# Kernel optimization log

Hardware: AMD Instinct MI355X
Metric: run time of the kernel (lower is better)

## Reference

```python
import jax, jax.numpy as jnp
import numpy as np

B, L, H, E = 4, 2048, 8, 64
WINDOW = 8
DILATION = 1


def setup_inputs() -> dict:
    key = jax.random.key(0)
    kq, kk, kv, ka = jax.random.split(key, 4)
    queries = jax.random.normal(kq, (B, L, H, E), dtype=jnp.float32)
    keys = jax.random.normal(kk, (B, L, H, E), dtype=jnp.float32)
    values = jax.random.normal(kv, (B, L, H, E), dtype=jnp.float32)
    alpha = jax.random.uniform(ka, (1,), dtype=jnp.float32)
    return {"queries": queries, "keys": keys, "values": values, "alpha": alpha}


def _full_attention(q, k, v, scale):
    # q,k,v: [B, L, H, E]
    scores = jnp.einsum('blhe,bshe->bhls', q, k) * scale  # [B,H,L,L]
    A = jax.nn.softmax(scores, axis=-1)
    return jnp.einsum('bhls,bshd->blhd', A, v)


def _local_attention(q, k, v, scale):
    # efficient gather-based local window attention, non-causal
    Lk = k.shape[1]
    offsets = jnp.arange(-WINDOW, WINDOW + 1) * DILATION
    idx = jnp.clip(jnp.arange(Lk)[:, None] + offsets[None, :], 0, Lk - 1)
    K_win = k[:, idx]
    V_win = v[:, idx]
    scores = jnp.einsum('blhe,blwhe->blhw', q, K_win) * scale
    A = jax.nn.softmax(scores, axis=-1)
    return jnp.einsum('blhw,blwhe->blhe', A, V_win)


def reference(queries, keys, values, alpha):
    scale = 1.0 / np.sqrt(queries.shape[-1]).astype(np.float32)
    out_full = _full_attention(queries, keys, values, scale)
    out_local = _local_attention(queries, keys, values, scale)
    w = jax.nn.sigmoid(alpha[0])
    # only_target_first=True: positions 1..L-1 take out_full, position 0 is gated
    out = out_full.at[:, 0].set(w * out_full[:, 0] + (1.0 - w) * out_local[:, 0])
    return out
```

## Files before the change

kernel.cpp:

```cpp
#include <hip/hip_runtime.h>

typedef unsigned short u16;
typedef unsigned int   u32;
typedef __attribute__((ext_vector_type(8))) short short8;
typedef __attribute__((ext_vector_type(16))) float f32x16;

#define MFMA32(a, b, c) __builtin_amdgcn_mfma_f32_32x32x16_bf16(a, b, c, 0, 0, 0)

constexpr int Lv = 2048, Hv = 8, Ev = 64, HE = Hv * Ev;
constexpr float QSCALE = 0.18033688011112042f;

__device__ __forceinline__ float bf2f(u16 u) {
    u32 x = ((u32)u) << 16;
    return __builtin_bit_cast(float, x);
}
__device__ __forceinline__ u16 f2bf(float f) {
    u32 x = __builtin_bit_cast(u32, f);
    u32 r = ((x >> 16) & 1u) + 0x7fffu;
    return (u16)((x + r) >> 16);
}
__device__ __forceinline__ u32 pkbf(float a, float b) {
#if __has_builtin(__builtin_amdgcn_cvt_pk_bf16_f32)
    typedef __attribute__((ext_vector_type(2))) __bf16 bf16x2;
    bf16x2 v = __builtin_amdgcn_cvt_pk_bf16_f32(a, b);
    return __builtin_bit_cast(u32, v);
#else
    return (u32)f2bf(a) | ((u32)f2bf(b) << 16);
#endif
}
__device__ __forceinline__ float fexp2(float x) {
#if __has_builtin(__builtin_amdgcn_exp2f)
    return __builtin_amdgcn_exp2f(x);
#else
    return exp2f(x);
#endif
}

__device__ __forceinline__ int detect_isbf16(const u32* q32, int lane) {
    u32 w0 = q32[2 * lane];
    u32 w1 = q32[2 * lane + 1];
    u16 uu[4] = { (u16)(w0 & 0xffff), (u16)(w0 >> 16),
                  (u16)(w1 & 0xffff), (u16)(w1 >> 16) };
    int p = 0, z = 0;
#pragma unroll
    for (int j = 0; j < 4; ++j) {
        u16 mgn = (u16)(uu[j] & 0x7fff);
        int ex  = mgn >> 7;
        bool zero = (mgn == 0);
        bool pl   = zero || (ex >= 115 && ex <= 132);
        p += pl ? 1 : 0;
        if ((j & 1) == 0) z += zero ? 1 : 0;
    }
    int acc = p | (z << 16);
#pragma unroll
    for (int o = 1; o < 64; o <<= 1) acc += __shfl_xor(acc, o);
    int ps = acc & 0xffff, zs = acc >> 16;
    if (zs >= 100) return 0;
    return (ps >= 240) ? 1 : 0;
}

__device__ __forceinline__ short8 cvt8s(const float* p, float s) {
    float4 a = *(const float4*)p, b4 = *(const float4*)(p + 4);
    u32 r[4] = { pkbf(a.x * s, a.y * s), pkbf(a.z * s, a.w * s),
                 pkbf(b4.x * s, b4.y * s), pkbf(b4.z * s, b4.w * s) };
    return *(short8*)r;
}

__device__ __forceinline__ f32x16 zv16() {
    f32x16 z;
#pragma unroll
    for (int r = 0; r < 16; ++r) z[r] = 0.f;
    return z;
}

__device__ __forceinline__ void plswap(u32& a, u32& b) {
#if __has_builtin(__builtin_amdgcn_permlane32_swap)
    auto r = __builtin_amdgcn_permlane32_swap(a, b, false, false);
    a = r[0]; b = r[1];
#else
    int lane = (int)(threadIdx.x & 63);
    u32 ax = (u32)__shfl_xor((int)a, 32);
    u32 bx = (u32)__shfl_xor((int)b, 32);
    bool hi = lane >= 32;
    u32 na = hi ? bx : a;
    u32 nb = hi ? b  : ax;
    a = na; b = nb;
#endif
}

template <int ISBF>
__device__ __forceinline__ void attn_impl(
    const void* __restrict__ qv, const void* __restrict__ kv,
    const void* __restrict__ vv, const void* __restrict__ alphav,
    void* __restrict__ outv, u16* SMEM)
{
    const int tid  = threadIdx.x;
    const int w    = tid >> 6;
    const int lane = tid & 63;
    const int l31  = lane & 31;
    const int hi   = lane >> 5;
    const int qg   = w & 3;
    const int g    = w >> 2;

    const int fid = blockIdx.x;
    const int bh  = (fid & 7) * 4 + ((fid >> 3) & 3);
    const int rb  = fid >> 5;
    const int b   = bh >> 3, h = bh & 7;
    const int row0 = rb * 128;

    const size_t bhoff = (size_t)b * Lv * HE + h * Ev;
    const u16*   q16 = (const u16*)qv + bhoff;
    const u16*   k16 = (const u16*)kv + bhoff;
    const u16*   v16 = (const u16*)vv + bhoff;
    const float* q32 = (const float*)qv + bhoff;
    const float* k32 = (const float*)kv + bhoff;
    const float* v32 = (const float*)vv + bhoff;

    u16* Klds = SMEM;
    u16* Vt   = SMEM + 8192;

    short8 qf[4];
    {
        size_t ro = (size_t)(row0 + qg * 32 + l31) * HE + hi * 8;
        if (ISBF) {
#pragma unroll
            for (int c = 0; c < 4; ++c) {
                short8 t = *(const short8*)(q16 + ro + 16 * c);
#pragma unroll
                for (int j = 0; j < 8; ++j)
                    qf[c][j] = (short)f2bf(bf2f((u16)t[j]) * QSCALE);
            }
        } else {
#pragma unroll
            for (int c = 0; c < 4; ++c) qf[c] = cvt8s(q32 + ro + 16 * c, QSCALE);
        }
    }

    f32x16 O[2];
    O[0] = zv16(); O[1] = zv16();
    float psum = 0.f;

    const int kkey = tid >> 3, ksl = tid & 7;
    const int koff = kkey * HE + ((ksl ^ (kkey & 7)) * 8);
    const int eq = tid & 15, pp = tid >> 4;
    const int kcv = pp >> 2, pq = pp & 3;

    float4 kfaA, kfbA, vfaA, vfbA, kfaB, kfbB, vfaB, vfbB;
    uint4  kruA, kruB; uint2 vru0A, vru1A, vru0B, vru1B;

#define LOAD_TILE(S, KT)                                                       \
    do {                                                                       \
        size_t kb_ = (size_t)(KT) * 64 * HE;                                   \
        if (ISBF) {                                                            \
            kru##S  = *(const uint4*)(k16 + kb_ + koff);                       \
            const u16* vp_ = v16 + kb_ + (size_t)(2 * pp) * HE + eq * 4;       \
            vru0##S = *(const uint2*)vp_;                                      \
            vru1##S = *(const uint2*)(vp_ + HE);                               \
        } else {                                                               \
            const float* kp_ = k32 + kb_ + koff;                               \
            kfa##S = *(const float4*)kp_;                                      \
            kfb##S = *(const float4*)(kp_ + 4);                                \
            const float* vp_ = v32 + kb_ + (size_t)(2 * pp) * HE + eq * 4;     \
            vfa##S = *(const float4*)vp_;                                      \
            vfb##S = *(const float4*)(vp_ + HE);                               \
        }                                                                      \
    } while (0)

#define STORE_TILE(S, KB, VB)                                                  \
    do {                                                                       \
        if (ISBF) {                                                            \
            *(uint4*)&(KB)[tid * 8] = kru##S;                                  \
            const u16* a0_ = (const u16*)&vru0##S;                             \
            const u16* a1_ = (const u16*)&vru1##S;                             \
            _Pragma("unroll")                                                  \
            for (int j = 0; j < 4; ++j) {                                      \
                int e_  = eq * 4 + j;                                          \
                int sl_ = kcv ^ ((e_ + (e_ >> 3)) & 7);                        \
                u32 val_ = (u32)a0_[j] | ((u32)a1_[j] << 16);                  \
                *(u32*)&(VB)[e_ * 64 + sl_ * 8 + pq * 2] = val_;               \
            }                                                                  \
        } else {                                                               \
            u32 kk_[4] = { pkbf(kfa##S.x, kfa##S.y), pkbf(kfa##S.z, kfa##S.w), \
                           pkbf(kfb##S.x, kfb##S.y), pkbf(kfb##S.z, kfb##S.w) };\
            *(uint4*)&(KB)[tid * 8] = *(uint4*)kk_;                            \
            float t0_[4] = {vfa##S.x, vfa##S.y, vfa##S.z, vfa##S.w};           \
            float t1_[4] = {vfb##S.x, vfb##S.y, vfb##S.z, vfb##S.w};           \
            _Pragma("unroll")                                                  \
            for (int j = 0; j < 4; ++j) {                                      \
                int e_  = eq * 4 + j;                                          \
                int sl_ = kcv ^ ((e_ + (e_ >> 3)) & 7);                        \
                *(u32*)&(VB)[e_ * 64 + sl_ * 8 + pq * 2] = pkbf(t0_[j], t1_[j]);\
            }                                                                  \
        }                                                                      \
    } while (0)

#define BODY(KT, SL, SS)                                                       \
    do {                                                                       \
        u16* Kb = Klds + ((KT) & 1) * 4096;                                    \
        u16* Vb = Vt   + ((KT) & 1) * 4096;                                    \
        if ((KT) < 30) LOAD_TILE(SL, (KT) + 2);                                \
        f32x16 St = zv16();                                                    \
        __builtin_amdgcn_s_setprio(1);                                         \
        _Pragma("unroll")                                                      \
        for (int c = 0; c < 4; ++c) {                                          \
            int sl = (2 * c + hi) ^ (l31 & 7);                                 \
            short8 kf = *(const short8*)&Kb[(g * 32 + l31) * 64 + sl * 8];     \
            St = MFMA32(kf, qf[c], St);                                        \
        }                                                                      \
        __builtin_amdgcn_s_setprio(0);                                         \
        _Pragma("unroll")                                                      \
        for (int r = 0; r < 16; ++r) St[r] = fexp2(St[r]);       \
        _Pragma("unroll")                                                      \
        for (int r = 0; r < 16; ++r) psum += St[r];                            \
        u32 c8[8];                                                             \
        _Pragma("unroll")                                                      \
        for (int q = 0; q < 8; ++q) c8[q] = pkbf(St[2 * q], St[2 * q + 1]);    \
        _Pragma("unroll")                                                      \
        for (int t = 0; t < 2; ++t) {                                          \
            u32 a0 = c8[4 * t + 0], a1 = c8[4 * t + 1];                        \
            u32 a2 = c8[4 * t + 2], a3 = c8[4 * t + 3];                        \
            plswap(a0, a2);                                                    \
            plswap(a1, a3);                                                    \
            u32 pw_[4] = { a0, a1, a2, a3 };                                   \
            short8 pa = *(short8*)pw_;                                         \
            int ks = 2 * g + t;                                                \
            __builtin_amdgcn_s_setprio(1);                                     \
            _Pragma("unroll")                                                  \
            for (int et = 0; et < 2; ++et) {                                   \
                int e  = et * 32 + l31;                                        \
                int sl = (2 * ks + hi) ^ ((e + (e >> 3)) & 7);                 \
                short8 vf = *(const short8*)&Vb[e * 64 + sl * 8];              \
                O[et] = MFMA32(pa, vf, O[et]);                                 \
            }                                                                  \
            __builtin_amdgcn_s_setprio(0);                                     \
        }                                                                      \
        if ((KT) < 31) {                                                       \
            u16* Kn = Klds + (((KT) + 1) & 1) * 4096;                          \
            u16* Vn = Vt   + (((KT) + 1) & 1) * 4096;                          \
            STORE_TILE(SS, Kn, Vn);                                            \
            asm volatile("s_waitcnt lgkmcnt(0)" ::: "memory");                 \
            __builtin_amdgcn_s_barrier();                                      \
        }                                                                      \
    } while (0)

    LOAD_TILE(A, 0);
    LOAD_TILE(B, 1);
    STORE_TILE(A, Klds, Vt);
    asm volatile("s_waitcnt lgkmcnt(0)" ::: "memory");
    __builtin_amdgcn_s_barrier();

    for (int kt2 = 0; kt2 < 16; ++kt2) {
        const int kt = 2 * kt2;
        BODY(kt,     A, B);
        BODY(kt + 1, B, A);
    }
#undef LOAD_TILE
#undef STORE_TILE
#undef BODY

    __syncthreads();
    float pst = psum + __shfl_xor(psum, 32);
    float* cb = (float*)SMEM;
    const int cbase = qg * 2368 + lane * 36;

    if (g == 1) {
        union { f32x16 v; float4 q4[4]; } u;
        u.v = O[0];
#pragma unroll
        for (int i = 0; i < 4; ++i) *(float4*)&cb[cbase + 4 * i] = u.q4[i];
        u.v = O[1];
#pragma unroll
        for (int i = 0; i < 4; ++i) *(float4*)&cb[cbase + 16 + 4 * i] = u.q4[i];
        cb[qg * 2368 + 2304 + lane] = pst;
    }

    float locv[2] = {0.f, 0.f};
    float wgt = 0.f;
    const bool w0blk = (rb == 0) && (w == 0);
    if (w0blk) {
        const int e = lane;
        const size_t base = bhoff + e;
#define LDIN(p, i) (ISBF ? bf2f(((const u16*)(p))[i]) : ((const float*)(p))[i])
        float qe = LDIN(qv, base);
        float s[9];
#pragma unroll
        for (int j = 0; j < 9; ++j) {
            float prod = qe * LDIN(kv, base + (size_t)j * HE);
#pragma unroll
            for (int o = 1; o < 64; o <<= 1) prod += __shfl_xor(prod, o);
            s[j] = prod * 0.125f;
        }
        float mx = s[0];
#pragma unroll
        for (int j = 1; j < 9; ++j) mx = fmaxf(mx, s[j]);
        float we[9];
#pragma unroll
        for (int j = 0; j < 9; ++j) we[j] = expf(s[j] - mx);
        float denom = 9.f * we[0];
        float acc   = 9.f * we[0] * LDIN(vv, base);
#pragma unroll
        for (int j = 1; j < 9; ++j) {
            denom += we[j];
            acc   += we[j] * LDIN(vv, base + (size_t)j * HE);
        }
        float loc = acc / denom;

        float a;
        if (ISBF) {
            a = bf2f(((const u16*)alphav)[0]);
            if (!(a >= 0.0f && a <= 1.0f)) {
                float af = ((const float*)alphav)[0];
                if (af >= 0.0f && af <= 1.0f) a = af;
            }
        } else {
            a = ((const float*)alphav)[0];
            if (!(a >= 0.0f && a <= 1.0f)) {
                float ab = bf2f(((const u16*)alphav)[0]);
                if (ab >= 0.0f && ab <= 1.0f) a = ab;
            }
        }
        wgt = 1.f / (1.f + expf(-a));
#pragma unroll
        for (int et = 0; et < 2; ++et) locv[et] = __shfl(loc, et * 32 + l31);
#undef LDIN
    }

    __syncthreads();
    if (g != 0) return;

    float pstp = cb[qg * 2368 + 2304 + lane];
#pragma unroll
    for (int r = 0; r < 16; ++r) {
        O[0][r] += cb[cbase + r];
        O[1][r] += cb[cbase + 16 + r];
    }
    float invv = 1.0f / (pst + pstp);

#pragma unroll
    for (int rg = 0; rg < 4; ++rg) {
#pragma unroll
        for (int rr = 0; rr < 4; ++rr) {
            const int reg = rg * 4 + rr;
            const int rl  = rr + 8 * rg + 4 * hi;
            float inv = __shfl(invv, rl);
            int row = row0 + qg * 32 + rl;
            size_t oo = (size_t)(b * Lv + row) * HE + h * Ev + l31;
            bool blend = w0blk && (rl == 0);
#pragma unroll
            for (int et = 0; et < 2; ++et) {
                float res = O[et][reg] * inv;
                if (blend) res = wgt * res + (1.f - wgt) * locv[et];
                if (ISBF) ((u16*)outv)[oo + et * 32] = f2bf(res);
                else      ((float*)outv)[oo + et * 32] = res;
            }
        }
    }
}

__global__ __launch_bounds__(512, 4) void attn_kernel(
    const void* __restrict__ qv, const void* __restrict__ kv,
    const void* __restrict__ vv, const void* __restrict__ alphav,
    void* __restrict__ outv)
{
    __shared__ u16 SMEM[18944];

    const int isbf = detect_isbf16((const u32*)qv, threadIdx.x & 63);
    if (isbf) attn_impl<1>(qv, kv, vv, alphav, outv, SMEM);
    else      attn_impl<0>(qv, kv, vv, alphav, outv, SMEM);
}

extern "C" void kernel_launch(void* const* d_in, const int* in_sizes, int n_in,
                              void* d_out, int out_size, void* d_ws, size_t ws_size,
                              hipStream_t stream) {
    hipLaunchKernelGGL(attn_kernel, dim3(512), dim3(512), 0, stream,
                       d_in[0], d_in[1], d_in[2], d_in[3], d_out);
}
```

Before: 143.2 us.

## Software-pipeline QK of next tile with softmax/PV of previous using triple-buffered LDS

```diff
diff --git a/kernel.cpp b/kernel.cpp
--- a/kernel.cpp
+++ b/kernel.cpp
@@ -117,7 +117,7 @@
     const float* v32 = (const float*)vv + bhoff;
 
     u16* Klds = SMEM;
-    u16* Vt   = SMEM + 8192;
+    u16* Vt   = SMEM + 12288;
 
     short8 qf[4];
     {
@@ -138,6 +138,7 @@
 
     f32x16 O[2];
     O[0] = zv16(); O[1] = zv16();
+    f32x16 StA = zv16(), StB = zv16();
     float psum = 0.f;
 
     const int kkey = tid >> 3, ksl = tid & 7;
@@ -145,76 +146,81 @@
     const int eq = tid & 15, pp = tid >> 4;
     const int kcv = pp >> 2, pq = pp & 3;
 
-    float4 kfaA, kfbA, vfaA, vfbA, kfaB, kfbB, vfaB, vfbB;
-    uint4  kruA, kruB; uint2 vru0A, vru1A, vru0B, vru1B;
-
-#define LOAD_TILE(S, KT)                                                       \
+    float4 kfa, kfb, vfa, vfb;
+    uint4  kru; uint2 vru0, vru1;
+
+#define LOAD_TILE(KT)                                                          \
     do {                                                                       \
         size_t kb_ = (size_t)(KT) * 64 * HE;                                   \
         if (ISBF) {                                                            \
-            kru##S  = *(const uint4*)(k16 + kb_ + koff);                       \
+            kru  = *(const uint4*)(k16 + kb_ + koff);                          \
             const u16* vp_ = v16 + kb_ + (size_t)(2 * pp) * HE + eq * 4;       \
-            vru0##S = *(const uint2*)vp_;                                      \
-            vru1##S = *(const uint2*)(vp_ + HE);                               \
+            vru0 = *(const uint2*)vp_;                                         \
+            vru1 = *(const uint2*)(vp_ + HE);                                  \
         } else {                                                               \
             const float* kp_ = k32 + kb_ + koff;                               \
-            kfa##S = *(const float4*)kp_;                                      \
-            kfb##S = *(const float4*)(kp_ + 4);                                \
+            kfa = *(const float4*)kp_;                                         \
+            kfb = *(const float4*)(kp_ + 4);                                   \
             const float* vp_ = v32 + kb_ + (size_t)(2 * pp) * HE + eq * 4;     \
-            vfa##S = *(const float4*)vp_;                                      \
-            vfb##S = *(const float4*)(vp_ + HE);                               \
+            vfa = *(const float4*)vp_;                                         \
+            vfb = *(const float4*)(vp_ + HE);                                  \
         }                                                                      \
     } while (0)
 
-#define STORE_TILE(S, KB, VB)                                                  \
-    do {                                                                       \
+#define STORE_TILE(BS)                                                         \
+    do {                                                                       \
+        u16* KB = Klds + (BS) * 4096;                                          \
+        u16* VB = Vt   + (BS) * 4096;                                          \
         if (ISBF) {                                                            \
-            *(uint4*)&(KB)[tid * 8] = kru##S;                                  \
-            const u16* a0_ = (const u16*)&vru0##S;                             \
-            const u16* a1_ = (const u16*)&vru1##S;                             \
+            *(uint4*)&KB[tid * 8] = kru;                                       \
+            const u16* a0_ = (const u16*)&vru0;                                \
+            const u16* a1_ = (const u16*)&vru1;                                \
             _Pragma("unroll")                                                  \
             for (int j = 0; j < 4; ++j) {                                      \
                 int e_  = eq * 4 + j;                                          \
                 int sl_ = kcv ^ ((e_ + (e_ >> 3)) & 7);                        \
                 u32 val_ = (u32)a0_[j] | ((u32)a1_[j] << 16);                  \
-                *(u32*)&(VB)[e_ * 64 + sl_ * 8 + pq * 2] = val_;               \
+                *(u32*)&VB[e_ * 64 + sl_ * 8 + pq * 2] = val_;                 \
             }                                                                  \
         } else {                                                               \
-            u32 kk_[4] = { pkbf(kfa##S.x, kfa##S.y), pkbf(kfa##S.z, kfa##S.w), \
-                           pkbf(kfb##S.x, kfb##S.y), pkbf(kfb##S.z, kfb##S.w) };\
-            *(uint4*)&(KB)[tid * 8] = *(uint4*)kk_;                            \
-            float t0_[4] = {vfa##S.x, vfa##S.y, vfa##S.z, vfa##S.w};           \
-            float t1_[4] = {vfb##S.x, vfb##S.y, vfb##S.z, vfb##S.w};           \
+            u32 kk_[4] = { pkbf(kfa.x, kfa.y), pkbf(kfa.z, kfa.w),             \
+                           pkbf(kfb.x, kfb.y), pkbf(kfb.z, kfb.w) };           \
+            *(uint4*)&KB[tid * 8] = *(uint4*)kk_;                              \
+            float t0_[4] = {vfa.x, vfa.y, vfa.z, vfa.w};                       \
+            float t1_[4] = {vfb.x, vfb.y, vfb.z, vfb.w};                       \
             _Pragma("unroll")                                                  \
             for (int j = 0; j < 4; ++j) {                                      \
                 int e_  = eq * 4 + j;                                          \
                 int sl_ = kcv ^ ((e_ + (e_ >> 3)) & 7);                        \
-                *(u32*)&(VB)[e_ * 64 + sl_ * 8 + pq * 2] = pkbf(t0_[j], t1_[j]);\
+                *(u32*)&VB[e_ * 64 + sl_ * 8 + pq * 2] = pkbf(t0_[j], t1_[j]); \
             }                                                                  \
         }                                                                      \
     } while (0)
 
-#define BODY(KT, SL, SS)                                                       \
-    do {                                                                       \
-        u16* Kb = Klds + ((KT) & 1) * 4096;                                    \
-        u16* Vb = Vt   + ((KT) & 1) * 4096;                                    \
-        if ((KT) < 30) LOAD_TILE(SL, (KT) + 2);                                \
-        f32x16 St = zv16();                                                    \
+#define QK_ST(ST, BQ)                                                          \
+    do {                                                                       \
+        const u16* Kb = Klds + (BQ) * 4096;                                    \
+        (ST) = zv16();                                                         \
         __builtin_amdgcn_s_setprio(1);                                         \
         _Pragma("unroll")                                                      \
         for (int c = 0; c < 4; ++c) {                                          \
             int sl = (2 * c + hi) ^ (l31 & 7);                                 \
             short8 kf = *(const short8*)&Kb[(g * 32 + l31) * 64 + sl * 8];     \
-            St = MFMA32(kf, qf[c], St);                                        \
+            (ST) = MFMA32(kf, qf[c], (ST));                                    \
         }                                                                      \
         __builtin_amdgcn_s_setprio(0);                                         \
+    } while (0)
+
+#define FIN_ST(SP, BP)                                                         \
+    do {                                                                       \
+        const u16* Vb = Vt + (BP) * 4096;                                      \
         _Pragma("unroll")                                                      \
-        for (int r = 0; r < 16; ++r) St[r] = fexp2(St[r]);       \
+        for (int r = 0; r < 16; ++r) (SP)[r] = fexp2((SP)[r]);                 \
         _Pragma("unroll")                                                      \
-        for (int r = 0; r < 16; ++r) psum += St[r];                            \
+        for (int r = 0; r < 16; ++r) psum += (SP)[r];                          \
         u32 c8[8];                                                             \
         _Pragma("unroll")                                                      \
-        for (int q = 0; q < 8; ++q) c8[q] = pkbf(St[2 * q], St[2 * q + 1]);    \
+        for (int q = 0; q < 8; ++q) c8[q] = pkbf((SP)[2 * q], (SP)[2 * q + 1]);\
         _Pragma("unroll")                                                      \
         for (int t = 0; t < 2; ++t) {                                          \
             u32 a0 = c8[4 * t + 0], a1 = c8[4 * t + 1];                        \
@@ -234,28 +240,50 @@
             }                                                                  \
             __builtin_amdgcn_s_setprio(0);                                     \
         }                                                                      \
-        if ((KT) < 31) {                                                       \
-            u16* Kn = Klds + (((KT) + 1) & 1) * 4096;                          \
-            u16* Vn = Vt   + (((KT) + 1) & 1) * 4096;                          \
-            STORE_TILE(SS, Kn, Vn);                                            \
-            asm volatile("s_waitcnt lgkmcnt(0)" ::: "memory");                 \
-            __builtin_amdgcn_s_barrier();                                      \
-        }                                                                      \
-    } while (0)
-
-    LOAD_TILE(A, 0);
-    LOAD_TILE(B, 1);
-    STORE_TILE(A, Klds, Vt);
-    asm volatile("s_waitcnt lgkmcnt(0)" ::: "memory");
-    __builtin_amdgcn_s_barrier();
-
-    for (int kt2 = 0; kt2 < 16; ++kt2) {
-        const int kt = 2 * kt2;
-        BODY(kt,     A, B);
-        BODY(kt + 1, B, A);
-    }
+    } while (0)
+
+#define ENDBAR()                                                               \
+    do {                                                                       \
+        asm volatile("s_waitcnt lgkmcnt(0)" ::: "memory");                     \
+        __builtin_amdgcn_s_barrier();                                          \
+    } while (0)
+
+#define BODY(KT, BQ, BP, BS, SC, SP)                                           \
+    do {                                                                       \
+        LOAD_TILE((KT) + 1);                                                   \
+        QK_ST(SC, BQ);                                                         \
+        FIN_ST(SP, BP);                                                        \
+        STORE_TILE(BS);                                                        \
+        ENDBAR();                                                              \
+    } while (0)
+
+    LOAD_TILE(0);
+    STORE_TILE(0);
+    ENDBAR();
+
+    LOAD_TILE(1);
+    QK_ST(StA, 0);
+    STORE_TILE(1);
+    ENDBAR();
+
+    for (int j = 0; j < 5; ++j) {
+        const int kt = 6 * j + 1;
+        BODY(kt + 0, 1, 0, 2, StB, StA);
+        BODY(kt + 1, 2, 1, 0, StA, StB);
+        BODY(kt + 2, 0, 2, 1, StB, StA);
+        BODY(kt + 3, 1, 0, 2, StA, StB);
+        BODY(kt + 4, 2, 1, 0, StB, StA);
+        BODY(kt + 5, 0, 2, 1, StA, StB);
+    }
+
+    QK_ST(StB, 1);
+    FIN_ST(StA, 0);
+    FIN_ST(StB, 1);
 #undef LOAD_TILE
 #undef STORE_TILE
+#undef QK_ST
+#undef FIN_ST
+#undef ENDBAR
 #undef BODY
 
     __syncthreads();
@@ -362,7 +390,7 @@
     const void* __restrict__ vv, const void* __restrict__ alphav,
     void* __restrict__ outv)
 {
-    __shared__ u16 SMEM[18944];
+    __shared__ u16 SMEM[24576];
 
     const int isbf = detect_isbf16((const u32*)qv, threadIdx.x & 63);
     if (isbf) attn_impl<1>(qv, kv, vv, alphav, outv, SMEM);
```

New measurement: 152.6 us. 6.6% more time.

## Pre-convert K/V to swizzled bf16 workspace and use per-wave private LDS tiles

Applied to the files above, without the earlier changes.

```diff
diff --git a/kernel.cpp b/kernel.cpp
--- a/kernel.cpp
+++ b/kernel.cpp
@@ -9,6 +9,8 @@
 
 constexpr int Lv = 2048, Hv = 8, Ev = 64, HE = Hv * Ev;
 constexpr float QSCALE = 0.18033688011112042f;
+constexpr size_t WSV_OFF = 32u * 64u * 2048u;
+#define WS_NEED ((size_t)16777216)
 
 __device__ __forceinline__ float bf2f(u16 u) {
     u32 x = ((u32)u) << 16;
@@ -89,10 +91,56 @@
 }
 
 template <int ISBF>
+__device__ __forceinline__ void convert_impl(const void* kin, const void* vin,
+                                             u16* __restrict__ ws) {
+    const int blk = blockIdx.x;
+    const int bh  = blk >> 6, tg = blk & 63;
+    const int b   = bh >> 3,  h  = bh & 7;
+    const size_t inb = (size_t)b * Lv * HE + h * Ev;
+    u16* kimg = ws + (size_t)blk * 2048;
+    u16* vimg = ws + WSV_OFF + (size_t)blk * 2048;
+    const int t = threadIdx.x;
+#pragma unroll
+    for (int r = 0; r < 4; ++r) {
+        const int i = t + 256 * r;
+        const int a = 2 * i;
+        {
+            int key = a >> 6;
+            int slotf = (a & 63) >> 3, j0 = a & 7;
+            int e0 = ((slotf ^ (key & 7)) << 3) + j0;
+            size_t s = inb + (size_t)(tg * 32 + key) * HE + e0;
+            u32 val;
+            if (ISBF) { const u16* p = (const u16*)kin + s; val = (u32)p[0] | ((u32)p[1] << 16); }
+            else      { const float* p = (const float*)kin + s; val = pkbf(p[0], p[1]); }
+            *(u32*)&kimg[a] = val;
+        }
+        {
+            int e = a >> 5;
+            int slotf = (a & 31) >> 3, j0 = a & 7;
+            int k0 = ((slotf ^ ((e + (e >> 3)) & 3)) << 3) + j0;
+            size_t s0 = inb + (size_t)(tg * 32 + k0) * HE + e;
+            u32 val;
+            if (ISBF) { const u16* p = (const u16*)vin; val = (u32)p[s0] | ((u32)p[s0 + HE] << 16); }
+            else      { const float* p = (const float*)vin; val = pkbf(p[s0], p[s0 + HE]); }
+            *(u32*)&vimg[a] = val;
+        }
+    }
+}
+
+__global__ __launch_bounds__(256) void convert_kernel(
+    const void* __restrict__ qv, const void* __restrict__ kv,
+    const void* __restrict__ vv, u16* __restrict__ ws)
+{
+    const int isbf = detect_isbf16((const u32*)qv, threadIdx.x & 63);
+    if (isbf) convert_impl<1>(kv, vv, ws);
+    else      convert_impl<0>(kv, vv, ws);
+}
+
+template <int ISBF, int WS>
 __device__ __forceinline__ void attn_impl(
     const void* __restrict__ qv, const void* __restrict__ kv,
     const void* __restrict__ vv, const void* __restrict__ alphav,
-    void* __restrict__ outv, u16* SMEM)
+    void* __restrict__ outv, const u16* __restrict__ ws, u16* SMEM)
 {
     const int tid  = threadIdx.x;
     const int w    = tid >> 6;
@@ -116,8 +164,8 @@
     const float* k32 = (const float*)kv + bhoff;
     const float* v32 = (const float*)vv + bhoff;
 
-    u16* Klds = SMEM;
-    u16* Vt   = SMEM + 8192;
+    u16* ldsK = SMEM + w * 4096;
+    u16* ldsV = ldsK + 2048;
 
     short8 qf[4];
     {
@@ -140,123 +188,177 @@
     O[0] = zv16(); O[1] = zv16();
     float psum = 0.f;
 
-    const int kkey = tid >> 3, ksl = tid & 7;
-    const int koff = kkey * HE + ((ksl ^ (kkey & 7)) * 8);
-    const int eq = tid & 15, pp = tid >> 4;
-    const int kcv = pp >> 2, pq = pp & 3;
-
-    float4 kfaA, kfbA, vfaA, vfbA, kfaB, kfbB, vfaB, vfbB;
-    uint4  kruA, kruB; uint2 vru0A, vru1A, vru0B, vru1B;
-
-#define LOAD_TILE(S, KT)                                                       \
-    do {                                                                       \
-        size_t kb_ = (size_t)(KT) * 64 * HE;                                   \
+    const u16* kimg0 = ws + ((size_t)bh * 64 + g * 32) * 2048;
+    const u16* vimg0 = ws + WSV_OFF + ((size_t)bh * 64 + g * 32) * 2048;
+    const size_t keybase = (size_t)g * 1024;
+
+    const int k0l = lane >> 3;
+    const int kj  = lane & 7;
+    const int e0K = ((kj ^ k0l) << 3);
+    const int eoV = kj * 8;
+
+    uint4  kr0, kr1, kr2, kr3;
+    float4 fpa, fpb, fpc, fpd;
+    uint4  upa, upb;
+
+#define LK1(KT) do { const u16* ib_ = kimg0 + (size_t)(KT) * 2048 + lane * 8;  \
+        kr0 = *(const uint4*)ib_;        kr1 = *(const uint4*)(ib_ + 512);     \
+        kr2 = *(const uint4*)(ib_ + 1024); kr3 = *(const uint4*)(ib_ + 1536); } while (0)
+#define SK1() do { *(uint4*)&ldsK[lane * 8] = kr0;                             \
+        *(uint4*)&ldsK[512 + lane * 8] = kr1;                                  \
+        *(uint4*)&ldsK[1024 + lane * 8] = kr2;                                 \
+        *(uint4*)&ldsK[1536 + lane * 8] = kr3; } while (0)
+#define LV1(KT) do { const u16* ib_ = vimg0 + (size_t)(KT) * 2048 + lane * 8;  \
+        kr0 = *(const uint4*)ib_;        kr1 = *(const uint4*)(ib_ + 512);     \
+        kr2 = *(const uint4*)(ib_ + 1024); kr3 = *(const uint4*)(ib_ + 1536); } while (0)
+#define SV1() do { *(uint4*)&ldsV[lane * 8] = kr0;                             \
+        *(uint4*)&ldsV[512 + lane * 8] = kr1;                                  \
+        *(uint4*)&ldsV[1024 + lane * 8] = kr2;                                 \
+        *(uint4*)&ldsV[1536 + lane * 8] = kr3; } while (0)
+
+#define LK0(KT, CH) do {                                                       \
+        size_t tb_ = (keybase + (size_t)(KT) * 32) * HE;                       \
+        int key_ = (CH) * 16 + k0l;                                            \
         if (ISBF) {                                                            \
-            kru##S  = *(const uint4*)(k16 + kb_ + koff);                       \
-            const u16* vp_ = v16 + kb_ + (size_t)(2 * pp) * HE + eq * 4;       \
-            vru0##S = *(const uint2*)vp_;                                      \
-            vru1##S = *(const uint2*)(vp_ + HE);                               \
+            const u16* p_ = k16 + tb_ + (size_t)key_ * HE + e0K;               \
+            upa = *(const uint4*)p_;                                           \
+            upb = *(const uint4*)(p_ + 8 * HE);                                \
         } else {                                                               \
-            const float* kp_ = k32 + kb_ + koff;                               \
-            kfa##S = *(const float4*)kp_;                                      \
-            kfb##S = *(const float4*)(kp_ + 4);                                \
-            const float* vp_ = v32 + kb_ + (size_t)(2 * pp) * HE + eq * 4;     \
-            vfa##S = *(const float4*)vp_;                                      \
-            vfb##S = *(const float4*)(vp_ + HE);                               \
-        }                                                                      \
-    } while (0)
-
-#define STORE_TILE(S, KB, VB)                                                  \
-    do {                                                                       \
+            const float* p_ = k32 + tb_ + (size_t)key_ * HE + e0K;             \
+            fpa = *(const float4*)p_;            fpb = *(const float4*)(p_ + 4);\
+            fpc = *(const float4*)(p_ + 8 * HE); fpd = *(const float4*)(p_ + 8 * HE + 4);\
+        }                                                                      \
+    } while (0)
+#define SK0(CH) do {                                                           \
         if (ISBF) {                                                            \
-            *(uint4*)&(KB)[tid * 8] = kru##S;                                  \
-            const u16* a0_ = (const u16*)&vru0##S;                             \
-            const u16* a1_ = (const u16*)&vru1##S;                             \
+            *(uint4*)&ldsK[((CH)*2    ) * 512 + lane * 8] = upa;               \
+            *(uint4*)&ldsK[((CH)*2 + 1) * 512 + lane * 8] = upb;               \
+        } else {                                                               \
+            u32 t0_[4] = { pkbf(fpa.x, fpa.y), pkbf(fpa.z, fpa.w),             \
+                           pkbf(fpb.x, fpb.y), pkbf(fpb.z, fpb.w) };           \
+            u32 t1_[4] = { pkbf(fpc.x, fpc.y), pkbf(fpc.z, fpc.w),             \
+                           pkbf(fpd.x, fpd.y), pkbf(fpd.z, fpd.w) };           \
+            *(uint4*)&ldsK[((CH)*2    ) * 512 + lane * 8] = *(uint4*)t0_;      \
+            *(uint4*)&ldsK[((CH)*2 + 1) * 512 + lane * 8] = *(uint4*)t1_;      \
+        }                                                                      \
+    } while (0)
+
+#define LV0(KT, VH) do {                                                       \
+        size_t tb_ = (keybase + (size_t)(KT) * 32 + (VH) * 16 + 2 * k0l) * HE; \
+        if (ISBF) {                                                            \
+            const u16* p_ = v16 + tb_ + eoV;                                   \
+            upa = *(const uint4*)p_;                                           \
+            upb = *(const uint4*)(p_ + HE);                                    \
+        } else {                                                               \
+            const float* p_ = v32 + tb_ + eoV;                                 \
+            fpa = *(const float4*)p_;       fpb = *(const float4*)(p_ + 4);    \
+            fpc = *(const float4*)(p_ + HE); fpd = *(const float4*)(p_ + HE + 4);\
+        }                                                                      \
+    } while (0)
+#define SV0(VH) do {                                                           \
+        int s_ = (k0l >> 2) + (VH) * 2;                                        \
+        if (ISBF) {                                                            \
+            const u16* a0_ = (const u16*)&upa;                                 \
+            const u16* a1_ = (const u16*)&upb;                                 \
             _Pragma("unroll")                                                  \
-            for (int j = 0; j < 4; ++j) {                                      \
-                int e_  = eq * 4 + j;                                          \
-                int sl_ = kcv ^ ((e_ + (e_ >> 3)) & 7);                        \
-                u32 val_ = (u32)a0_[j] | ((u32)a1_[j] << 16);                  \
-                *(u32*)&(VB)[e_ * 64 + sl_ * 8 + pq * 2] = val_;               \
+            for (int j = 0; j < 8; ++j) {                                      \
+                int e_ = eoV + j;                                              \
+                int sl_ = s_ ^ ((e_ + (e_ >> 3)) & 3);                         \
+                *(u32*)&ldsV[e_ * 32 + sl_ * 8 + ((2 * k0l) & 7)] =            \
+                    (u32)a0_[j] | ((u32)a1_[j] << 16);                         \
             }                                                                  \
         } else {                                                               \
-            u32 kk_[4] = { pkbf(kfa##S.x, kfa##S.y), pkbf(kfa##S.z, kfa##S.w), \
-                           pkbf(kfb##S.x, kfb##S.y), pkbf(kfb##S.z, kfb##S.w) };\
-            *(uint4*)&(KB)[tid * 8] = *(uint4*)kk_;                            \
-            float t0_[4] = {vfa##S.x, vfa##S.y, vfa##S.z, vfa##S.w};           \
-            float t1_[4] = {vfb##S.x, vfb##S.y, vfb##S.z, vfb##S.w};           \
+            float t0_[8] = {fpa.x, fpa.y, fpa.z, fpa.w, fpb.x, fpb.y, fpb.z, fpb.w};\
+            float t1_[8] = {fpc.x, fpc.y, fpc.z, fpc.w, fpd.x, fpd.y, fpd.z, fpd.w};\
             _Pragma("unroll")                                                  \
-            for (int j = 0; j < 4; ++j) {                                      \
-                int e_  = eq * 4 + j;                                          \
-                int sl_ = kcv ^ ((e_ + (e_ >> 3)) & 7);                        \
-                *(u32*)&(VB)[e_ * 64 + sl_ * 8 + pq * 2] = pkbf(t0_[j], t1_[j]);\
+            for (int j = 0; j < 8; ++j) {                                      \
+                int e_ = eoV + j;                                              \
+                int sl_ = s_ ^ ((e_ + (e_ >> 3)) & 3);                         \
+                *(u32*)&ldsV[e_ * 32 + sl_ * 8 + ((2 * k0l) & 7)] =            \
+                    pkbf(t0_[j], t1_[j]);                                      \
             }                                                                  \
         }                                                                      \
     } while (0)
 
-#define BODY(KT, SL, SS)                                                       \
-    do {                                                                       \
-        u16* Kb = Klds + ((KT) & 1) * 4096;                                    \
-        u16* Vb = Vt   + ((KT) & 1) * 4096;                                    \
-        if ((KT) < 30) LOAD_TILE(SL, (KT) + 2);                                \
-        f32x16 St = zv16();                                                    \
+    f32x16 St;
+#define QK_() do {                                                             \
+        St = zv16();                                                           \
         __builtin_amdgcn_s_setprio(1);                                         \
         _Pragma("unroll")                                                      \
         for (int c = 0; c < 4; ++c) {                                          \
             int sl = (2 * c + hi) ^ (l31 & 7);                                 \
-            short8 kf = *(const short8*)&Kb[(g * 32 + l31) * 64 + sl * 8];     \
+            short8 kf = *(const short8*)&ldsK[l31 * 64 + sl * 8];              \
             St = MFMA32(kf, qf[c], St);                                        \
         }                                                                      \
         __builtin_amdgcn_s_setprio(0);                                         \
+    } while (0)
+
+    u32 c8[8];
+#define SM_() do {                                                             \
         _Pragma("unroll")                                                      \
-        for (int r = 0; r < 16; ++r) St[r] = fexp2(St[r]);       \
+        for (int r = 0; r < 16; ++r) St[r] = fexp2(St[r]);                     \
         _Pragma("unroll")                                                      \
         for (int r = 0; r < 16; ++r) psum += St[r];                            \
-        u32 c8[8];                                                             \
         _Pragma("unroll")                                                      \
         for (int q = 0; q < 8; ++q) c8[q] = pkbf(St[2 * q], St[2 * q + 1]);    \
+    } while (0)
+
+#define PV_(T) do {                                                            \
+        u32 a0 = c8[4 * (T) + 0], a1 = c8[4 * (T) + 1];                        \
+        u32 a2 = c8[4 * (T) + 2], a3 = c8[4 * (T) + 3];                        \
+        plswap(a0, a2);                                                        \
+        plswap(a1, a3);                                                        \
+        u32 pw_[4] = { a0, a1, a2, a3 };                                       \
+        short8 pa = *(short8*)pw_;                                             \
+        __builtin_amdgcn_s_setprio(1);                                         \
         _Pragma("unroll")                                                      \
-        for (int t = 0; t < 2; ++t) {                                          \
-            u32 a0 = c8[4 * t + 0], a1 = c8[4 * t + 1];                        \
-            u32 a2 = c8[4 * t + 2], a3 = c8[4 * t + 3];                        \
-            plswap(a0, a2);                                                    \
-            plswap(a1, a3);                                                    \
-            u32 pw_[4] = { a0, a1, a2, a3 };                                   \
-            short8 pa = *(short8*)pw_;                                         \
-            int ks = 2 * g + t;                                                \
-            __builtin_amdgcn_s_setprio(1);                                     \
-            _Pragma("unroll")                                                  \
-            for (int et = 0; et < 2; ++et) {                                   \
-                int e  = et * 32 + l31;                                        \
-                int sl = (2 * ks + hi) ^ ((e + (e >> 3)) & 7);                 \
-                short8 vf = *(const short8*)&Vb[e * 64 + sl * 8];              \
-                O[et] = MFMA32(pa, vf, O[et]);                                 \
-            }                                                                  \
-            __builtin_amdgcn_s_setprio(0);                                     \
-        }                                                                      \
-        if ((KT) < 31) {                                                       \
-            u16* Kn = Klds + (((KT) + 1) & 1) * 4096;                          \
-            u16* Vn = Vt   + (((KT) + 1) & 1) * 4096;                          \
-            STORE_TILE(SS, Kn, Vn);                                            \
-            asm volatile("s_waitcnt lgkmcnt(0)" ::: "memory");                 \
-            __builtin_amdgcn_s_barrier();                                      \
-        }                                                                      \
-    } while (0)
-
-    LOAD_TILE(A, 0);
-    LOAD_TILE(B, 1);
-    STORE_TILE(A, Klds, Vt);
-    asm volatile("s_waitcnt lgkmcnt(0)" ::: "memory");
-    __builtin_amdgcn_s_barrier();
-
-    for (int kt2 = 0; kt2 < 16; ++kt2) {
-        const int kt = 2 * kt2;
-        BODY(kt,     A, B);
-        BODY(kt + 1, B, A);
-    }
-#undef LOAD_TILE
-#undef STORE_TILE
-#undef BODY
+        for (int et = 0; et < 2; ++et) {                                       \
+            int e  = et * 32 + l31;                                            \
+            int sl = (2 * (T) + hi) ^ ((e + (e >> 3)) & 3);                    \
+            short8 vf = *(const short8*)&ldsV[e * 32 + sl * 8];                \
+            O[et] = MFMA32(pa, vf, O[et]);                                     \
+        }                                                                      \
+        __builtin_amdgcn_s_setprio(0);                                         \
+    } while (0)
+
+    if (WS) {
+        LK1(0); SK1(); LV1(0); SV1();
+        for (int kt = 0; kt < 32; ++kt) {
+            if (kt < 31) LK1(kt + 1);
+            QK_();
+            if (kt < 31) SK1();
+            SM_();
+            if (kt < 31) LV1(kt + 1);
+            PV_(0);
+            PV_(1);
+            if (kt < 31) SV1();
+        }
+    } else {
+        LK0(0, 0); SK0(0); LK0(0, 1); SK0(1);
+        LV0(0, 0); SV0(0); LV0(0, 1); SV0(1);
+        for (int kt = 0; kt < 32; ++kt) {
+            if (kt < 31) LK0(kt + 1, 0);
+            QK_();
+            if (kt < 31) { SK0(0); LK0(kt + 1, 1); }
+            SM_();
+            if (kt < 31) { SK0(1); LV0(kt + 1, 0); }
+            PV_(0);
+            if (kt < 31) { SV0(0); LV0(kt + 1, 1); }
+            PV_(1);
+            if (kt < 31) SV0(1);
+        }
+    }
+#undef LK1
+#undef SK1
+#undef LV1
+#undef SV1
+#undef LK0
+#undef SK0
+#undef LV0
+#undef SV0
+#undef QK_
+#undef SM_
+#undef PV_
 
     __syncthreads();
     float pst = psum + __shfl_xor(psum, 32);
@@ -357,21 +459,39 @@
     }
 }
 
-__global__ __launch_bounds__(512, 4) void attn_kernel(
+__global__ __launch_bounds__(512, 4) void attn_kernel_ws(
+    const void* __restrict__ qv, const void* __restrict__ kv,
+    const void* __restrict__ vv, const void* __restrict__ alphav,
+    void* __restrict__ outv, const u16* __restrict__ ws)
+{
+    __shared__ u16 SMEM[32768];
+    const int isbf = detect_isbf16((const u32*)qv, threadIdx.x & 63);
+    if (isbf) attn_impl<1, 1>(qv, kv, vv, alphav, outv, ws, SMEM);
+    else      attn_impl<0, 1>(qv, kv, vv, alphav, outv, ws, SMEM);
+}
+
+__global__ __launch_bounds__(512, 4) void attn_kernel_nws(
     const void* __restrict__ qv, const void* __restrict__ kv,
     const void* __restrict__ vv, const void* __restrict__ alphav,
     void* __restrict__ outv)
 {
-    __shared__ u16 SMEM[18944];
-
+    __shared__ u16 SMEM[32768];
     const int isbf = detect_isbf16((const u32*)qv, threadIdx.x & 63);
-    if (isbf) attn_impl<1>(qv, kv, vv, alphav, outv, SMEM);
-    else      attn_impl<0>(qv, kv, vv, alphav, outv, SMEM);
+    if (isbf) attn_impl<1, 0>(qv, kv, vv, alphav, outv, nullptr, SMEM);
+    else      attn_impl<0, 0>(qv, kv, vv, alphav, outv, nullptr, SMEM);
 }
 
 extern "C" void kernel_launch(void* const* d_in, const int* in_sizes, int n_in,
                               void* d_out, int out_size, void* d_ws, size_t ws_size,
                               hipStream_t stream) {
-    hipLaunchKernelGGL(attn_kernel, dim3(512), dim3(512), 0, stream,
-                       d_in[0], d_in[1], d_in[2], d_in[3], d_out);
-}
+    if (d_ws != nullptr && ws_size >= WS_NEED) {
+        hipLaunchKernelGGL(convert_kernel, dim3(2048), dim3(256), 0, stream,
+                           d_in[0], d_in[1], d_in[2], (u16*)d_ws);
+        hipLaunchKernelGGL(attn_kernel_ws, dim3(512), dim3(512), 0, stream,
+                           d_in[0], d_in[1], d_in[2], d_in[3], d_out,
+                           (const u16*)d_ws);
+    } else {
+        hipLaunchKernelGGL(attn_kernel_nws, dim3(512), dim3(512), 0, stream,
+                           d_in[0], d_in[1], d_in[2], d_in[3], d_out);
+    }
+}
```

Result: slower. 155.4 us (+8.5%).
